# Optimization experiments

Measured on AMD Instinct MI355X. Metric: run time of the kernel, lower is better.

## Reference

```python
import jax, jax.numpy as jnp
import numpy as np

H_DIM = 1024
GATE_DIM = 128


def setup_inputs() -> dict:
    key = jax.random.key(0)
    ks = jax.random.split(key, 7)
    B, L = 32, 2048
    bound_g = 1.0 / np.sqrt(GATE_DIM)
    bound_l = 1.0 / np.sqrt(GATE_DIM)
    return {
        "x": jax.random.normal(ks[0], (B, L, H_DIM), dtype=jnp.float32),
        # GRUCell params (PyTorch layout: rows ordered [r; z; n])
        "weight_ih": jax.random.uniform(ks[1], (3 * GATE_DIM, H_DIM), minval=-bound_g, maxval=bound_g, dtype=jnp.float32),
        "weight_hh": jax.random.uniform(ks[2], (3 * GATE_DIM, GATE_DIM), minval=-bound_g, maxval=bound_g, dtype=jnp.float32),
        "bias_ih": jax.random.uniform(ks[3], (3 * GATE_DIM,), minval=-bound_g, maxval=bound_g, dtype=jnp.float32),
        "bias_hh": jax.random.uniform(ks[4], (3 * GATE_DIM,), minval=-bound_g, maxval=bound_g, dtype=jnp.float32),
        # output linear (gate_dim -> 1)
        "lin_w": jax.random.uniform(ks[5], (1, GATE_DIM), minval=-bound_l, maxval=bound_l, dtype=jnp.float32),
        "lin_b": jax.random.uniform(ks[6], (1,), minval=-bound_l, maxval=bound_l, dtype=jnp.float32),
    }


def reference(x, weight_ih, weight_hh, bias_ih, bias_hh, lin_w, lin_b):
    """Faithful to the original PingHead.forward: `s` is never updated, so every
    timestep runs the GRUCell against a ZERO hidden state. weight_hh @ h == 0,
    leaving only bias_hh contributions. This lets us vectorize over (B, L)."""
    G = GATE_DIM
    # input projection for all gates: (B, L, 3G)
    gi = jnp.einsum('blh,gh->blg', x, weight_ih) + bias_ih
    i_r, i_z, i_n = gi[..., :G], gi[..., G:2 * G], gi[..., 2 * G:]
    b_hr, b_hz, b_hn = bias_hh[:G], bias_hh[G:2 * G], bias_hh[2 * G:]
    r = jax.nn.sigmoid(i_r + b_hr)
    z = jax.nn.sigmoid(i_z + b_hz)
    n = jnp.tanh(i_n + r * b_hn)
    h = (1.0 - z) * n  # + z * 0 (hidden state is always zero)
    # linear(gate_dim -> 1), squeeze last dim -> (B, L)
    out = jnp.einsum('blg,og->blo', h, lin_w) + lin_b
    return out[..., 0]
```

## Files before the change

### kernel.cpp

```cpp
#include <hip/hip_runtime.h>

#define H_DIM   1024
#define G_DIM   128
#define N_DIM   384
#define M_TOTAL 65536
#define BM      64

typedef _Float16 half8  __attribute__((ext_vector_type(8)));
typedef _Float16 half4  __attribute__((ext_vector_type(4)));
typedef __fp16   fp16x2 __attribute__((ext_vector_type(2)));
typedef float    f32x4  __attribute__((ext_vector_type(4)));

__device__ __forceinline__ float fast_sigmoid(float v) {
    return 1.0f / (1.0f + __expf(-v));
}
__device__ __forceinline__ float fast_tanh(float v) {
    return 1.0f - 2.0f / (__expf(2.0f * v) + 1.0f);
}

__device__ __forceinline__ half4 cvt4(f32x4 v) {
    fp16x2 p0 = __builtin_amdgcn_cvt_pkrtz(v[0], v[1]);
    fp16x2 p1 = __builtin_amdgcn_cvt_pkrtz(v[2], v[3]);
    half4 h;
    h[0] = (_Float16)p0[0]; h[1] = (_Float16)p0[1];
    h[2] = (_Float16)p1[0]; h[3] = (_Float16)p1[1];
    return h;
}

__global__ __launch_bounds__(256) void prep_w_kernel(const float* __restrict__ w,
                                                     _Float16* __restrict__ wf) {
    int gid  = blockIdx.x * 256 + threadIdx.x;
    int lane = gid & 63;
    int fid  = gid >> 6;
    int ktg  = fid & 31;
    int ct   = fid >> 5;
    int col  = ct * 16 + (lane & 15);
    int kb   = ktg * 32 + (lane >> 4) * 8;
    const f32x4* src = (const f32x4*)(w + (size_t)col * H_DIM + kb);
    f32x4 v0 = src[0], v1 = src[1];
    half8 h;
    #pragma unroll
    for (int j = 0; j < 4; ++j) { h[j] = (_Float16)v0[j]; h[4 + j] = (_Float16)v1[j]; }
    *(half8*)(wf + (size_t)gid * 8) = h;
}

#define FENCE() asm volatile("" ::: "memory")
#define WAITV(N)    { FENCE(); __builtin_amdgcn_s_waitcnt(0x0F70 | (N)); FENCE(); }
#define WAITLGKM0() { FENCE(); __builtin_amdgcn_s_waitcnt(0xC07F); FENCE(); }
#define BARRW()     { WAITLGKM0(); __builtin_amdgcn_s_barrier(); FENCE(); }

__global__ __launch_bounds__(512, 4) void ping_main_kernel(
    const float* __restrict__ x, const _Float16* __restrict__ wf,
    const float* __restrict__ bias_ih, const float* __restrict__ bias_hh,
    const float* __restrict__ lin_w, const float* __restrict__ lin_b,
    float* __restrict__ out)
{
    __shared__ _Float16 shX[2 * 2048];
    __shared__ float sh_out[BM];

    const int t    = threadIdx.x;
    const int lane = t & 63;
    const int wv   = t >> 6;
    const int ln   = lane & 15;
    const int quad = lane >> 4;

    if (t < BM) sh_out[t] = 0.0f;

    const size_t row0 = (size_t)blockIdx.x * BM;

    const int drow = wv * 8 + (lane >> 3);
    const int dcol = (lane & 7) * 4;
    const float* xsrc = x + (row0 + drow) * (size_t)H_DIM + dcol;
    _Float16* wdst = &shX[drow * 32 + dcol];

    const char* aBase = (const char*)&shX[0] + ln * 64 + quad * 16;

    const _Float16* pb[3];
    #pragma unroll
    for (int i = 0; i < 3; ++i)
        pb[i] = wf + (size_t)((wv + 8 * i) * 32) * 512 + lane * 8;

    f32x4 acc[3][4];
    #pragma unroll
    for (int i = 0; i < 3; ++i)
        #pragma unroll
        for (int rt = 0; rt < 4; ++rt)
            acc[i][rt] = (f32x4){0.f, 0.f, 0.f, 0.f};

    f32x4 g[2];
    half8 bf[2][3];

    g[0] = *(const f32x4*)(xsrc);
    g[1] = *(const f32x4*)(xsrc + 32);
    #pragma unroll
    for (int i = 0; i < 3; ++i) {
        bf[0][i] = *(const half8*)(pb[i]);
        bf[1][i] = *(const half8*)(pb[i] + 512);
    }
    WAITV(7);
    *(half4*)(wdst) = cvt4(g[0]);
    BARRW();

#define STEP(KB, PAR, DO_PF, WAITN, DO_STAGE) { \
    if (DO_PF) g[PAR] = *(const f32x4*)(xsrc + (size_t)((KB) + 2) * 32); \
    _Pragma("unroll") \
    for (int rt = 0; rt < 4; ++rt) { \
        half8 afr = *(const half8*)(aBase + (PAR) * 4096 + rt * 1024); \
        _Pragma("unroll") \
        for (int i = 0; i < 3; ++i) \
            acc[i][rt] = __builtin_amdgcn_mfma_f32_16x16x32_f16(afr, bf[PAR][i], acc[i][rt], 0, 0, 0); \
    } \
    if (DO_PF) { \
        _Pragma("unroll") \
        for (int i = 0; i < 3; ++i) \
            bf[PAR][i] = *(const half8*)(pb[i] + (size_t)((KB) + 2) * 512); \
    } \
    if (DO_STAGE) { \
        WAITV(WAITN); \
        *(half4*)(wdst + (((PAR) ^ 1) * 2048)) = cvt4(g[(PAR) ^ 1]); \
    } \
    BARRW(); }

    for (int kb = 0; kb < 30; kb += 2) {
        STEP(kb + 0, 0, true, 7, true);
        STEP(kb + 1, 1, true, 7, true);
    }
    STEP(30, 0, false, 3, true);
    STEP(31, 1, false, 0, false);

    const int g_col = 16 * wv + ln;
    const float b_ir = bias_ih[g_col];
    const float b_iz = bias_ih[G_DIM + g_col];
    const float b_in = bias_ih[2 * G_DIM + g_col];
    const float b_hr = bias_hh[g_col];
    const float b_hz = bias_hh[G_DIM + g_col];
    const float b_hn = bias_hh[2 * G_DIM + g_col];
    const float lw   = lin_w[g_col];

    #pragma unroll
    for (int rt = 0; rt < 4; ++rt) {
        #pragma unroll
        for (int reg = 0; reg < 4; ++reg) {
            const float r = fast_sigmoid(acc[0][rt][reg] + b_ir + b_hr);
            const float z = fast_sigmoid(acc[1][rt][reg] + b_iz + b_hz);
            const float n = fast_tanh(acc[2][rt][reg] + b_in + r * b_hn);
            float v = lw * (1.0f - z) * n;
            v += __shfl_xor(v, 1);
            v += __shfl_xor(v, 2);
            v += __shfl_xor(v, 4);
            v += __shfl_xor(v, 8);
            if (ln == 0) atomicAdd(&sh_out[rt * 16 + quad * 4 + reg], v);
        }
    }

    __syncthreads();
    if (t < BM) out[row0 + t] = sh_out[t] + lin_b[0];
}

extern "C" void kernel_launch(void* const* d_in, const int* in_sizes, int n_in,
                              void* d_out, int out_size, void* d_ws, size_t ws_size,
                              hipStream_t stream) {
    const float* x      = (const float*)d_in[0];
    const float* w_ih   = (const float*)d_in[1];
    const float* b_ih   = (const float*)d_in[3];
    const float* b_hh   = (const float*)d_in[4];
    const float* lin_w  = (const float*)d_in[5];
    const float* lin_b  = (const float*)d_in[6];
    float* out          = (float*)d_out;
    _Float16* wf        = (_Float16*)d_ws;

    hipLaunchKernelGGL(prep_w_kernel, dim3((N_DIM / 16) * 32 * 64 / 256), dim3(256), 0, stream,
                       w_ih, wf);
    hipLaunchKernelGGL(ping_main_kernel, dim3(M_TOTAL / BM), dim3(512), 0, stream,
                       x, wf, b_ih, b_hh, lin_w, lin_b, out);
}
```

Before: 406.5 us.

## Deepen x staging to four LDS buffers and barrier every other k-step

```diff
diff --git a/kernel.cpp b/kernel.cpp
--- a/kernel.cpp
+++ b/kernel.cpp
@@ -45,7 +45,6 @@
 }
 
 #define FENCE() asm volatile("" ::: "memory")
-#define WAITV(N)    { FENCE(); __builtin_amdgcn_s_waitcnt(0x0F70 | (N)); FENCE(); }
 #define WAITLGKM0() { FENCE(); __builtin_amdgcn_s_waitcnt(0xC07F); FENCE(); }
 #define BARRW()     { WAITLGKM0(); __builtin_amdgcn_s_barrier(); FENCE(); }
 
@@ -55,7 +54,7 @@
     const float* __restrict__ lin_w, const float* __restrict__ lin_b,
     float* __restrict__ out)
 {
-    __shared__ _Float16 shX[2 * 2048];
+    __shared__ _Float16 shX[4 * 2048];
     __shared__ float sh_out[BM];
 
     const int t    = threadIdx.x;
@@ -87,46 +86,54 @@
         for (int rt = 0; rt < 4; ++rt)
             acc[i][rt] = (f32x4){0.f, 0.f, 0.f, 0.f};
 
-    f32x4 g[2];
+    f32x4 g[4];
     half8 bf[2][3];
 
     g[0] = *(const f32x4*)(xsrc);
     g[1] = *(const f32x4*)(xsrc + 32);
+    g[2] = *(const f32x4*)(xsrc + 64);
+    g[3] = *(const f32x4*)(xsrc + 96);
     #pragma unroll
     for (int i = 0; i < 3; ++i) {
         bf[0][i] = *(const half8*)(pb[i]);
         bf[1][i] = *(const half8*)(pb[i] + 512);
     }
-    WAITV(7);
-    *(half4*)(wdst) = cvt4(g[0]);
+    *(half4*)(wdst)        = cvt4(g[0]);
+    *(half4*)(wdst + 2048) = cvt4(g[1]);
+    g[0] = *(const f32x4*)(xsrc + 128);
     BARRW();
 
-#define STEP(KB, PAR, DO_PF, WAITN, DO_STAGE) { \
-    if (DO_PF) g[PAR] = *(const f32x4*)(xsrc + (size_t)((KB) + 2) * 32); \
+#define STEP(K, DO_G, DO_B, DO_S, DO_BAR) { \
     _Pragma("unroll") \
     for (int rt = 0; rt < 4; ++rt) { \
-        half8 afr = *(const half8*)(aBase + (PAR) * 4096 + rt * 1024); \
+        half8 afr = *(const half8*)(aBase + ((K) & 3) * 4096 + rt * 1024); \
         _Pragma("unroll") \
         for (int i = 0; i < 3; ++i) \
-            acc[i][rt] = __builtin_amdgcn_mfma_f32_16x16x32_f16(afr, bf[PAR][i], acc[i][rt], 0, 0, 0); \
+            acc[i][rt] = __builtin_amdgcn_mfma_f32_16x16x32_f16(afr, bf[(K) & 1][i], acc[i][rt], 0, 0, 0); \
     } \
-    if (DO_PF) { \
+    if (DO_G) g[((K) + 1) & 3] = *(const f32x4*)(xsrc + (size_t)((K) + 5) * 32); \
+    if (DO_B) { \
         _Pragma("unroll") \
         for (int i = 0; i < 3; ++i) \
-            bf[PAR][i] = *(const half8*)(pb[i] + (size_t)((KB) + 2) * 512); \
+            bf[(K) & 1][i] = *(const half8*)(pb[i] + (size_t)((K) + 2) * 512); \
     } \
-    if (DO_STAGE) { \
-        WAITV(WAITN); \
-        *(half4*)(wdst + (((PAR) ^ 1) * 2048)) = cvt4(g[(PAR) ^ 1]); \
-    } \
-    BARRW(); }
+    if (DO_S) *(half4*)(wdst + (((K) + 2) & 3) * 2048) = cvt4(g[((K) + 2) & 3]); \
+    if (DO_BAR) BARRW(); }
 
-    for (int kb = 0; kb < 30; kb += 2) {
-        STEP(kb + 0, 0, true, 7, true);
-        STEP(kb + 1, 1, true, 7, true);
+    for (int kb = 0; kb < 24; kb += 4) {
+        STEP(kb + 0, true, true, true, false);
+        STEP(kb + 1, true, true, true, true);
+        STEP(kb + 2, true, true, true, false);
+        STEP(kb + 3, true, true, true, true);
     }
-    STEP(30, 0, false, 3, true);
-    STEP(31, 1, false, 0, false);
+    STEP(24, true,  true,  true,  false);
+    STEP(25, true,  true,  true,  true);
+    STEP(26, true,  true,  true,  false);
+    STEP(27, false, true,  true,  true);
+    STEP(28, false, true,  true,  false);
+    STEP(29, false, true,  true,  true);
+    STEP(30, false, false, false, false);
+    STEP(31, false, false, false, false);
 
     const int g_col = 16 * wv + ln;
     const float b_ir = bias_ih[g_col];
```

New measurement: 392.1 us. -3.5%, faster.
